# Performance work log

Measured on AMD Instinct MI355X. Metric: run time of the kernel, lower is better.

The kernel has to match this reference:

```python
import jax, jax.numpy as jnp
import numpy as np

B, T, C, H, TT = 8, 1024, 512, 8, 4  # batch, seq, n_embd, n_head, total_timestep
D = C // H


def setup_inputs() -> dict:
    key = jax.random.key(0)
    ks = jax.random.split(key, 4)
    s = 1.0 / np.sqrt(C)
    return {
        "x": jax.random.normal(ks[0], (B, T, C), jnp.float32),
        "padding_mask": jax.random.bernoulli(ks[1], 0.1, (TT, T)),  # bool
        "W_qkv": jax.random.normal(ks[2], (C, 3 * C), jnp.float32) * s,
        "b_qkv": jnp.zeros((3 * C,), jnp.float32),
        "W_proj": jax.random.normal(ks[3], (C, C), jnp.float32) * s,
        "b_proj": jnp.zeros((C,), jnp.float32),
    }


def reference(x, padding_mask, W_qkv, b_qkv, W_proj, b_proj):
    # fused QKV projection
    qkv = x @ W_qkv + b_qkv                       # [B,T,3C]
    q, k, v = jnp.split(qkv, 3, axis=-1)
    q = q.reshape(B, T, H, D)
    k = k.reshape(B, T, H, D)
    v = v.reshape(B, T, H, D)

    # mask: causal OR padding (True = attend), replicating torch semantics
    causal = jnp.tril(jnp.ones((T, T), bool))                 # [T,T]
    m = causal[None] | padding_mask[:, :, None]               # [TT,T,T]
    mask = jnp.broadcast_to(m[None], (B // TT, TT, T, T)).reshape(B, 1, T, T)

    scores = jnp.einsum("bqhd,bkhd->bhqk", q, k) * (1.0 / np.sqrt(D))
    scores = jnp.where(mask, scores, jnp.float32(-1e30))
    attn = jax.nn.softmax(scores, axis=-1)                    # [B,H,T,T]
    y = jnp.einsum("bhqk,bkhd->bqhd", attn, v).reshape(B, T, C)
    return y @ W_proj + b_proj
```

## Files before the change

### kernel.cpp

```cpp
#include <hip/hip_runtime.h>
#include <hip/hip_bf16.h>

#define BB 8
#define TT_ 4
#define TSEQ 1024
#define CEMB 512
#define NH 8
#define HD 64

typedef __attribute__((ext_vector_type(8))) short bf16x8;
typedef __attribute__((ext_vector_type(4))) float f32x4;
typedef __attribute__((ext_vector_type(16))) float f32x16;

#define AS1 __attribute__((address_space(1)))
#define AS3 __attribute__((address_space(3)))

__device__ __forceinline__ void gload_lds16(const void* g, void* l) {
  __builtin_amdgcn_global_load_lds((const AS1 unsigned int*)g, (AS3 unsigned int*)l, 16, 0, 0);
}

__device__ __forceinline__ short f2b(float f) {
  union { float f; unsigned u; } v; v.f = f;
  unsigned r = v.u + 0x7FFFu + ((v.u >> 16) & 1u);
  return (short)(r >> 16);
}

__device__ __forceinline__ unsigned pack2(float a, float b) {
  unsigned r;
  asm("v_cvt_pk_bf16_f32 %0, %1, %2" : "=v"(r) : "v"(a), "v"(b));
  return r;
}

__global__ __launch_bounds__(256) void k_prep(
    const float* __restrict__ x, short* __restrict__ xb,
    const float* __restrict__ w0, short* __restrict__ t0,
    const float* __restrict__ w1, short* __restrict__ t1)
{
  __shared__ float tsh[64][65];
  const int bid = blockIdx.x;

  if (bid < 2048) {
    const int i = bid * 256 + threadIdx.x;
    float4 v0 = ((const float4*)x)[i * 2];
    float4 v1 = ((const float4*)x)[i * 2 + 1];
    union { unsigned u[4]; bf16x8 v; } o;
    o.u[0] = pack2(v0.x, v0.y); o.u[1] = pack2(v0.z, v0.w);
    o.u[2] = pack2(v1.x, v1.y); o.u[3] = pack2(v1.z, v1.w);
    ((bf16x8*)xb)[i] = o.v;
    return;
  }

  const int z = (bid >= 2240);
  const int tile = z ? (bid - 2240) : (bid - 2048);
  const int ntx = z ? 8 : 24;
  const float* w = z ? w1 : w0;
  short* wt = z ? t1 : t0;
  const int N = z ? 512 : 1536, K = 512;
  const int tx = threadIdx.x & 15, ty = threadIdx.x >> 4;
  const int n0 = (tile % ntx) * 64, k0 = (tile / ntx) * 64;
#pragma unroll
  for (int i = 0; i < 4; ++i) {
    int kr = i * 16 + ty;
    float4 v = *(const float4*)&w[(size_t)(k0 + kr) * N + n0 + tx * 4];
    tsh[tx * 4 + 0][kr] = v.x; tsh[tx * 4 + 1][kr] = v.y;
    tsh[tx * 4 + 2][kr] = v.z; tsh[tx * 4 + 3][kr] = v.w;
  }
  __syncthreads();
#pragma unroll
  for (int i = 0; i < 4; ++i) {
    int nr = i * 16 + ty;
    short4 o;
    o.x = f2b(tsh[nr][tx * 4 + 0]); o.y = f2b(tsh[nr][tx * 4 + 1]);
    o.z = f2b(tsh[nr][tx * 4 + 2]); o.w = f2b(tsh[nr][tx * 4 + 3]);
    *(short4*)&wt[(size_t)(n0 + nr) * K + k0 + tx * 4] = o;
  }
}

__global__ __launch_bounds__(256) void k_gemm0(
    const short* __restrict__ A, const short* __restrict__ Bt,
    const float* __restrict__ bias,
    short* __restrict__ qb, short* __restrict__ kb, short* __restrict__ vtb,
    const void* __restrict__ pin, int* __restrict__ pme,
    int* __restrict__ perm, int* __restrict__ chunk_nkt)
{
  __shared__ short As[3][128 * 32];
  __shared__ short Bs[3][128 * 32];

  if (blockIdx.x == 768) {
    __shared__ int bad_f32, any_f32, bad_i32, any_i32, bad_u16, any_u16;
    if (threadIdx.x == 0) { bad_f32 = any_f32 = bad_i32 = any_i32 = bad_u16 = any_u16 = 0; }
    __syncthreads();
    const unsigned char* pb = (const unsigned char*)pin;
    const float* pf = (const float*)pin;
    const int* pi = (const int*)pin;
    const unsigned short* ph = (const unsigned short*)pin;
    for (int i = threadIdx.x; i < 1024; i += 256) {
      float fv = pf[i];
      if (fv != 0.0f && fv != 1.0f) bad_f32 = 1;
      if (fv == 1.0f) any_f32 = 1;
      int iv = pi[i];
      if (iv != 0 && iv != 1) bad_i32 = 1;
      if (iv == 1) any_i32 = 1;
    }
    for (int i = threadIdx.x; i < 2048; i += 256) {
      unsigned short hv = ph[i];
      if (hv != 0 && hv != 0x3F80u && hv != 0x3C00u) bad_u16 = 1;
      if (hv == 0x3F80u || hv == 0x3C00u) any_u16 = 1;
    }
    __syncthreads();
    int mode = 3;
    if (!bad_f32 && any_f32) mode = 0;
    else if (!bad_i32 && any_i32) mode = 1;
    else if (!bad_u16 && any_u16) mode = 2;
    for (int i = threadIdx.x; i < TT_ * TSEQ; i += 256) {
      int v;
      if (mode == 0)      v = (pf[i] != 0.0f);
      else if (mode == 1) v = (pi[i] != 0);
      else if (mode == 2) v = (ph[i] != 0);
      else                v = (pb[i] != 0);
      pme[i] = v;
    }
    __syncthreads();
    const int w = threadIdx.x >> 6, lane = threadIdx.x & 63;
    {
      const int* rowp = pme + w * 1024;
      unsigned long long bal[16];
      int npm = 0;
#pragma unroll
      for (int g = 0; g < 16; ++g) {
        bal[g] = __ballot(rowp[g * 64 + lane] != 0);
        npm += __popcll(bal[g]);
      }
      int off_non = 0, off_pm = 1024 - npm;
#pragma unroll
      for (int g = 0; g < 16; ++g) {
        unsigned long long m = bal[g];
        int below = __popcll(m & ((1ull << lane) - 1ull));
        int ispm = (int)((m >> lane) & 1ull);
        int pos = ispm ? (off_pm + below) : (off_non + lane - below);
        perm[w * 1024 + pos] = g * 64 + lane;
        int c = __popcll(m);
        off_pm += c; off_non += 64 - c;
      }
    }
    __syncthreads();
    {
      const int tt = w, c = (lane >> 3) & 7, seg = lane & 7;
      int mx = 0;
#pragma unroll
      for (int i = 0; i < 16; ++i) {
        int q = perm[tt * 1024 + c * 128 + seg * 16 + i];
        int need = pme[tt * 1024 + q] ? 16 : ((q >> 6) + 1);
        mx = mx > need ? mx : need;
      }
#pragma unroll
      for (int s = 1; s < 8; s <<= 1) {
        int o = __shfl_xor(mx, s, 64);
        mx = mx > o ? mx : o;
      }
      if (seg == 0) chunk_nkt[tt * 8 + c] = mx;
    }
    return;
  }

  const int tid = threadIdx.x, lane = tid & 63, w = tid >> 6;
  const int wm = w >> 1, wn = w & 1;
  const int idp = (blockIdx.x & 7) * 96 + (blockIdx.x >> 3);
  const int n0 = (idp % 12) * 128, m0 = (idp / 12) * 128;
  f32x4 acc[4][4] = {};
  const char* Abase = (const char*)A + (size_t)m0 * 1024;
  const char* Bbase = (const char*)Bt + (size_t)n0 * 1024;
  const int rowL = w * 16 + (lane >> 2);
  const int colB = (lane & 3) * 16;

  auto stage = [&](int buf, int k0) {
#pragma unroll
    for (int is = 0; is < 2; ++is) {
      int row = is * 64 + rowL;
      gload_lds16(Abase + (size_t)row * 1024 + (size_t)(k0 * 2 + colB),
                  (char*)As[buf] + is * 4096 + w * 1024);
      gload_lds16(Bbase + (size_t)row * 1024 + (size_t)(k0 * 2 + colB),
                  (char*)Bs[buf] + is * 4096 + w * 1024);
    }
  };

  stage(0, 0);
  stage(1, 32);
#pragma unroll
  for (int it = 0; it < 16; ++it) {
    if (it < 15) asm volatile("s_waitcnt vmcnt(4)\n\ts_barrier" ::: "memory");
    else         asm volatile("s_waitcnt vmcnt(0)\n\ts_barrier" ::: "memory");
    if (it + 2 < 16) stage((it + 2) % 3, (it + 2) * 32);
    const short* Ab = As[it % 3];
    const short* Bb = Bs[it % 3];
    bf16x8 a[4], bfr[4];
#pragma unroll
    for (int mf = 0; mf < 4; ++mf)
      a[mf] = *(const bf16x8*)&Ab[(wm * 64 + mf * 16 + (lane & 15)) * 32 + (lane >> 4) * 8];
#pragma unroll
    for (int nf = 0; nf < 4; ++nf)
      bfr[nf] = *(const bf16x8*)&Bb[(wn * 64 + nf * 16 + (lane & 15)) * 32 + (lane >> 4) * 8];
#pragma unroll
    for (int mf = 0; mf < 4; ++mf)
#pragma unroll
      for (int nf = 0; nf < 4; ++nf)
        acc[mf][nf] = __builtin_amdgcn_mfma_f32_16x16x32_bf16(a[mf], bfr[nf], acc[mf][nf], 0, 0, 0);
  }

#pragma unroll
  for (int nf = 0; nf < 4; ++nf) {
    const int n_g = n0 + wn * 64 + nf * 16 + (lane & 15);
    const float bv = bias[n_g];
    const int which = n_g >> 9;
    const int c = n_g & 511;
    const int h = c >> 6, d = c & 63;
    const float qsc = (which == 0) ? 0.18033688011112043f : 1.0f;
#pragma unroll
    for (int mf = 0; mf < 4; ++mf) {
      const int mb = m0 + wm * 64 + mf * 16 + ((lane >> 4) << 2);
      const int b = mb >> 10, t0 = mb & 1023;
      const int b8h = b * NH + h;
      if (which == 2) {
        short4 pk;
        pk.x = f2b(acc[mf][nf][0] + bv);
        pk.y = f2b(acc[mf][nf][1] + bv);
        pk.z = f2b(acc[mf][nf][2] + bv);
        pk.w = f2b(acc[mf][nf][3] + bv);
        *(short4*)&vtb[((size_t)b8h * HD + d) * TSEQ + t0] = pk;
      } else {
        short* dst = (which == 0) ? qb : kb;
        size_t base = ((size_t)b8h * TSEQ + t0) * HD + d;
#pragma unroll
        for (int r = 0; r < 4; ++r)
          dst[base + (size_t)r * HD] = f2b((acc[mf][nf][r] + bv) * qsc);
      }
    }
  }
}

__global__ __launch_bounds__(256) void k_gemm1(
    const short* __restrict__ A, const short* __restrict__ Bt,
    const float* __restrict__ bias, float* __restrict__ fout)
{
  __shared__ short As[3][64 * 32];
  __shared__ short Bs[3][128 * 32];
  const int tid = threadIdx.x, lane = tid & 63, w = tid >> 6;
  const int wm = w >> 1, wn = w & 1;
  const int idp = (blockIdx.x & 7) * 64 + (blockIdx.x >> 3);
  const int n0 = (idp & 3) * 128, m0 = (idp >> 2) * 64;
  f32x4 acc[2][4] = {};
  const char* Abase = (const char*)A + (size_t)m0 * 1024;
  const char* Bbase = (const char*)Bt + (size_t)n0 * 1024;
  const int rowL = tid >> 2;
  const int colB = (tid & 3) * 16;

  auto stage = [&](int buf, int k0) {
    gload_lds16(Abase + (size_t)rowL * 1024 + (size_t)(k0 * 2 + colB),
                (char*)As[buf] + w * 1024);
#pragma unroll
    for (int is = 0; is < 2; ++is) {
      int row = is * 64 + rowL;
      gload_lds16(Bbase + (size_t)row * 1024 + (size_t)(k0 * 2 + colB),
                  (char*)Bs[buf] + is * 4096 + w * 1024);
    }
  };

  stage(0, 0);
  stage(1, 32);
#pragma unroll
  for (int it = 0; it < 16; ++it) {
    if (it < 15) asm volatile("s_waitcnt vmcnt(3)\n\ts_barrier" ::: "memory");
    else         asm volatile("s_waitcnt vmcnt(0)\n\ts_barrier" ::: "memory");
    if (it + 2 < 16) stage((it + 2) % 3, (it + 2) * 32);
    const short* Ab = As[it % 3];
    const short* Bb = Bs[it % 3];
    bf16x8 a[2], bfr[4];
#pragma unroll
    for (int mf = 0; mf < 2; ++mf)
      a[mf] = *(const bf16x8*)&Ab[(wm * 32 + mf * 16 + (lane & 15)) * 32 + (lane >> 4) * 8];
#pragma unroll
    for (int nf = 0; nf < 4; ++nf)
      bfr[nf] = *(const bf16x8*)&Bb[(wn * 64 + nf * 16 + (lane & 15)) * 32 + (lane >> 4) * 8];
#pragma unroll
    for (int mf = 0; mf < 2; ++mf)
#pragma unroll
      for (int nf = 0; nf < 4; ++nf)
        acc[mf][nf] = __builtin_amdgcn_mfma_f32_16x16x32_bf16(a[mf], bfr[nf], acc[mf][nf], 0, 0, 0);
  }

#pragma unroll
  for (int nf = 0; nf < 4; ++nf) {
    const int n_g = n0 + wn * 64 + nf * 16 + (lane & 15);
    const float bv = bias[n_g];
#pragma unroll
    for (int mf = 0; mf < 2; ++mf) {
      const int mb = m0 + wm * 32 + mf * 16 + ((lane >> 4) << 2);
#pragma unroll
      for (int r = 0; r < 4; ++r)
        fout[(size_t)(mb + r) * 512 + n_g] = acc[mf][nf][r] + bv;
    }
  }
}

__device__ __forceinline__ void pv_step(
    f32x16 p, int sub, int hi, int lq, const char* Vsb, f32x16& o0, f32x16& o1)
{
  unsigned P2[8];
#pragma unroll
  for (int i = 0; i < 8; ++i) P2[i] = pack2(p[2 * i], p[2 * i + 1]);
  unsigned e0 = __shfl_xor(hi ? P2[0] : P2[2], 32, 64);
  unsigned e1 = __shfl_xor(hi ? P2[1] : P2[3], 32, 64);
  unsigned e2 = __shfl_xor(hi ? P2[4] : P2[6], 32, 64);
  unsigned e3 = __shfl_xor(hi ? P2[5] : P2[7], 32, 64);
  union { unsigned u[4]; bf16x8 v; } f0, f1;
  f0.u[0] = hi ? e0 : P2[0]; f0.u[1] = hi ? e1 : P2[1];
  f0.u[2] = hi ? P2[2] : e0; f0.u[3] = hi ? P2[3] : e1;
  f1.u[0] = hi ? e2 : P2[4]; f1.u[1] = hi ? e3 : P2[5];
  f1.u[2] = hi ? P2[6] : e2; f1.u[3] = hi ? P2[7] : e3;
  __builtin_amdgcn_s_setprio(1);
#pragma unroll
  for (int dt = 0; dt < 2; ++dt) {
    int row = dt * 32 + lq;
    bf16x8 v0 = *(const bf16x8*)(Vsb + row * 128 + ((4 * sub + hi) ^ (row & 7)) * 16);
    bf16x8 v1 = *(const bf16x8*)(Vsb + row * 128 + ((4 * sub + 2 + hi) ^ (row & 7)) * 16);
    f32x16& o = dt ? o1 : o0;
    o = __builtin_amdgcn_mfma_f32_32x32x16_bf16(v0, f0.v, o, 0, 0, 0);
    o = __builtin_amdgcn_mfma_f32_32x32x16_bf16(v1, f1.v, o, 0, 0, 0);
  }
  __builtin_amdgcn_s_setprio(0);
}

__global__ __launch_bounds__(512) void k_attn(
    const short* __restrict__ qg, const short* __restrict__ kg,
    const short* __restrict__ vtg, const int* __restrict__ pme,
    const int* __restrict__ perm, const int* __restrict__ chunk_nkt,
    short* __restrict__ yb)
{
  __shared__ char smem[65536];
  const int tid = threadIdx.x, lane = tid & 63, w = tid >> 6;
  const int g = w >> 2;
  const int hi = lane >> 5, lq = lane & 31;
  const int id = blockIdx.x;
  const int bh = id & 63, b = bh >> 3, h = bh & 7, tt = b & 3;
  const int p = id >> 6;
  const int chunk = (p < 4) ? (7 - p) : (p - 4);
  const char* Qb = (const char*)(qg + (size_t)bh * TSEQ * HD);
  const char* Kb = (const char*)(kg + (size_t)bh * TSEQ * HD);
  const char* Vb = (const char*)(vtg + (size_t)bh * HD * TSEQ);

  const int stg_row = ((w & 3) << 3) + (lane >> 3);
  const int stg_cl = (lane & 7) ^ ((lane >> 3) & 7);

  auto stage = [&](int buf, int kt) {
#pragma unroll
    for (int is = 0; is < 2; ++is) {
      int row = is * 32 + stg_row;
      gload_lds16(Kb + (size_t)(kt * 64 + row) * 128 + stg_cl * 16,
                  smem + buf * 8192 + is * 4096 + (w & 3) * 1024);
      gload_lds16(Vb + (size_t)row * 2048 + kt * 128 + stg_cl * 16,
                  smem + 32768 + buf * 8192 + is * 4096 + (w & 3) * 1024);
    }
  };

  const int nkt = chunk_nkt[tt * 8 + chunk];
  const int q_g = perm[tt * 1024 + chunk * 128 + (w & 3) * 32 + lq];
  const int pmrow = pme[tt * TSEQ + q_g];

  if (g < nkt) stage(g * 2, g);

  int wmq = q_g, wnq = q_g;
#pragma unroll
  for (int s = 1; s < 64; s <<= 1) {
    wmq = max(wmq, __shfl_xor(wmq, s, 64));
    wnq = min(wnq, __shfl_xor(wnq, s, 64));
  }
  const int whaspm = __any(pmrow != 0);

  bf16x8 qf[4];
#pragma unroll
  for (int dk = 0; dk < 4; ++dk)
    qf[dk] = *(const bf16x8*)(Qb + (size_t)q_g * 128 + dk * 32 + hi * 16);

  float mrun = -1e30f, lrun = 0.0f;
  f32x16 o0 = {}, o1 = {};

  const int niter = (nkt + 1) >> 1;
  for (int i = 0; i < niter; ++i) {
    asm volatile("s_waitcnt vmcnt(0)" ::: "memory");
    __builtin_amdgcn_s_barrier();
    const int kt = 2 * i + g;
    if (kt + 2 < nkt) stage(g * 2 + ((i + 1) & 1), kt + 2);

    const int kb_ = kt * 64;
    if (kt < nkt && (kb_ <= wmq || whaspm)) {
      const char* Ksb = smem + (g * 2 + (i & 1)) * 8192;
      const char* Vsb = smem + 32768 + (g * 2 + (i & 1)) * 8192;

      f32x16 s0 = {}, s1 = {};
      __builtin_amdgcn_s_setprio(1);
#pragma unroll
      for (int dk = 0; dk < 4; ++dk) {
        int row0 = lq, row1 = 32 + lq;
        bf16x8 kf0 = *(const bf16x8*)(Ksb + row0 * 128 + ((2 * dk + hi) ^ (row0 & 7)) * 16);
        bf16x8 kf1 = *(const bf16x8*)(Ksb + row1 * 128 + ((2 * dk + hi) ^ (row1 & 7)) * 16);
        s0 = __builtin_amdgcn_mfma_f32_32x32x16_bf16(kf0, qf[dk], s0, 0, 0, 0);
        s1 = __builtin_amdgcn_mfma_f32_32x32x16_bf16(kf1, qf[dk], s1, 0, 0, 0);
      }
      __builtin_amdgcn_s_setprio(0);

      if (kb_ + 63 <= wnq) {
      } else if (kb_ > wmq) {
#pragma unroll
        for (int r = 0; r < 16; ++r) {
          s0[r] = pmrow ? s0[r] : -1e30f;
          s1[r] = pmrow ? s1[r] : -1e30f;
        }
      } else {
#pragma unroll
        for (int r = 0; r < 16; ++r) {
          int crow = (r & 3) + 8 * (r >> 2) + 4 * hi;
          s0[r] = ((kb_ + crow <= q_g) || pmrow) ? s0[r] : -1e30f;
          s1[r] = ((kb_ + 32 + crow <= q_g) || pmrow) ? s1[r] : -1e30f;
        }
      }

      float tm[16];
#pragma unroll
      for (int r = 0; r < 16; ++r) tm[r] = fmaxf(s0[r], s1[r]);
#pragma unroll
      for (int st = 8; st >= 1; st >>= 1)
#pragma unroll
        for (int r = 0; r < 8; ++r)
          if (r < st) tm[r] = fmaxf(tm[r], tm[r + st]);
      float mx = fmaxf(tm[0], __shfl_xor(tm[0], 32, 64));
      if (!__all(mx <= mrun + 8.0f)) {
        float nm = fmaxf(mrun, mx);
        float sc = __builtin_amdgcn_exp2f(mrun - nm);
        lrun *= sc;
#pragma unroll
        for (int r = 0; r < 16; ++r) { o0[r] *= sc; o1[r] *= sc; }
        mrun = nm;
      }
#pragma unroll
      for (int r = 0; r < 16; ++r) s0[r] = __builtin_amdgcn_exp2f(s0[r] - mrun);
#pragma unroll
      for (int r = 0; r < 16; ++r) s1[r] = __builtin_amdgcn_exp2f(s1[r] - mrun);
      float ts[16];
#pragma unroll
      for (int r = 0; r < 16; ++r) ts[r] = s0[r] + s1[r];
#pragma unroll
      for (int st = 8; st >= 1; st >>= 1)
#pragma unroll
        for (int r = 0; r < 8; ++r)
          if (r < st) ts[r] = ts[r] + ts[r + st];
      lrun += ts[0] + __shfl_xor(ts[0], 32, 64);

      pv_step(s0, 0, hi, lq, Vsb, o0, o1);
      pv_step(s1, 1, hi, lq, Vsb, o0, o1);
    }
  }

  __syncthreads();
  float* mg = (float*)smem;
  const int idx = (w & 3) * 64 + lane;
  if (g == 1) {
    mg[idx * 34 + 0] = mrun;
    mg[idx * 34 + 1] = lrun;
#pragma unroll
    for (int j = 0; j < 16; ++j) mg[idx * 34 + 2 + j] = o0[j];
#pragma unroll
    for (int j = 0; j < 16; ++j) mg[idx * 34 + 18 + j] = o1[j];
  }
  __syncthreads();
  if (g == 0) {
    const float mB = mg[idx * 34 + 0], lB = mg[idx * 34 + 1];
    const float m = fmaxf(mrun, mB);
    const float wa = __builtin_amdgcn_exp2f(mrun - m);
    const float wb = __builtin_amdgcn_exp2f(mB - m);
    const float linv = 1.0f / (lrun * wa + lB * wb);
    const float fa = wa * linv, fb = wb * linv;
    short* yrow = yb + ((size_t)b * TSEQ + q_g) * CEMB + h * HD;
#pragma unroll
    for (int dt = 0; dt < 2; ++dt) {
      const f32x16& o = dt ? o1 : o0;
      const int ob = dt ? 18 : 2;
#pragma unroll
      for (int gg = 0; gg < 4; ++gg) {
        short4 pk;
        pk.x = f2b(o[4 * gg + 0] * fa + mg[idx * 34 + ob + 4 * gg + 0] * fb);
        pk.y = f2b(o[4 * gg + 1] * fa + mg[idx * 34 + ob + 4 * gg + 1] * fb);
        pk.z = f2b(o[4 * gg + 2] * fa + mg[idx * 34 + ob + 4 * gg + 2] * fb);
        pk.w = f2b(o[4 * gg + 3] * fa + mg[idx * 34 + ob + 4 * gg + 3] * fb);
        *(short4*)(yrow + dt * 32 + 8 * gg + 4 * hi) = pk;
      }
    }
  }
}

extern "C" void kernel_launch(void* const* d_in, const int* in_sizes, int n_in,
                              void* d_out, int out_size, void* d_ws, size_t ws_size,
                              hipStream_t stream) {
  const float* x     = (const float*)d_in[0];
  const void*  pmask = d_in[1];
  const float* Wqkv  = (const float*)d_in[2];
  const float* bqkv  = (const float*)d_in[3];
  const float* Wproj = (const float*)d_in[4];
  const float* bproj = (const float*)d_in[5];
  float* out = (float*)d_out;
  char* ws = (char*)d_ws;

  const size_t OFF_XB   = 0;
  const size_t OFF_WQT  = 8388608;
  const size_t OFF_WPT  = 9961472;
  const size_t OFF_Q    = 10485760;
  const size_t OFF_K    = 18874368;
  const size_t OFF_VT   = 27262976;
  const size_t OFF_Y    = 35651584;
  const size_t OFF_PM   = 44040192;
  const size_t OFF_PERM = 44056576;
  const size_t OFF_CNKT = 44072960;
  const size_t NEED     = 44073984;
  if (ws_size < NEED) return;

  short* xb  = (short*)(ws + OFF_XB);
  short* wqT = (short*)(ws + OFF_WQT);
  short* wpT = (short*)(ws + OFF_WPT);
  short* qb  = (short*)(ws + OFF_Q);
  short* kb  = (short*)(ws + OFF_K);
  short* vtb = (short*)(ws + OFF_VT);
  short* yb  = (short*)(ws + OFF_Y);
  int*   pme = (int*)(ws + OFF_PM);
  int*   prm = (int*)(ws + OFF_PERM);
  int*   cnk = (int*)(ws + OFF_CNKT);

  k_prep<<<dim3(2304), dim3(256), 0, stream>>>(x, xb, Wqkv, wqT, Wproj, wpT);
  k_gemm0<<<dim3(769), dim3(256), 0, stream>>>(xb, wqT, bqkv, qb, kb, vtb,
                                               pmask, pme, prm, cnk);
  k_attn<<<dim3(512), dim3(512), 0, stream>>>(qb, kb, vtb, pme, prm, cnk, yb);
  k_gemm1<<<dim3(512), dim3(256), 0, stream>>>(yb, wpT, bproj, out);
}
```

Measured before the change: 85.79 us.

## Move mask preprocessing to prep kernel, enlarge proj GEMM tile, stage attention output

Mask decoding, permutation and chunk-bound computation move from an extra block of the QKV GEMM into an extra block of the prep kernel, so the GEMM grid no longer carries a straggler block. The output projection GEMM switches from 64x128 to 128x128 tiles with half as many blocks, trading fewer blocks for more reuse per block. In attention, the chunk schedule becomes strictly descending, and outputs are staged in LDS then written as coalesced 16-byte rows using the permutation. The LDS staging adds a barrier, and the larger tiles leave fewer blocks to spread across CUs.

```diff
diff --git a/kernel.cpp b/kernel.cpp
--- a/kernel.cpp
+++ b/kernel.cpp
@@ -34,7 +34,9 @@
 __global__ __launch_bounds__(256) void k_prep(
     const float* __restrict__ x, short* __restrict__ xb,
     const float* __restrict__ w0, short* __restrict__ t0,
-    const float* __restrict__ w1, short* __restrict__ t1)
+    const float* __restrict__ w1, short* __restrict__ t1,
+    const void* __restrict__ pin, int* __restrict__ pme,
+    int* __restrict__ perm, int* __restrict__ chunk_nkt)
 {
   __shared__ float tsh[64][65];
   const int bid = blockIdx.x;
@@ -50,119 +52,117 @@
     return;
   }
 
-  const int z = (bid >= 2240);
-  const int tile = z ? (bid - 2240) : (bid - 2048);
-  const int ntx = z ? 8 : 24;
-  const float* w = z ? w1 : w0;
-  short* wt = z ? t1 : t0;
-  const int N = z ? 512 : 1536, K = 512;
-  const int tx = threadIdx.x & 15, ty = threadIdx.x >> 4;
-  const int n0 = (tile % ntx) * 64, k0 = (tile / ntx) * 64;
-#pragma unroll
-  for (int i = 0; i < 4; ++i) {
-    int kr = i * 16 + ty;
-    float4 v = *(const float4*)&w[(size_t)(k0 + kr) * N + n0 + tx * 4];
-    tsh[tx * 4 + 0][kr] = v.x; tsh[tx * 4 + 1][kr] = v.y;
-    tsh[tx * 4 + 2][kr] = v.z; tsh[tx * 4 + 3][kr] = v.w;
-  }
-  __syncthreads();
-#pragma unroll
-  for (int i = 0; i < 4; ++i) {
-    int nr = i * 16 + ty;
-    short4 o;
-    o.x = f2b(tsh[nr][tx * 4 + 0]); o.y = f2b(tsh[nr][tx * 4 + 1]);
-    o.z = f2b(tsh[nr][tx * 4 + 2]); o.w = f2b(tsh[nr][tx * 4 + 3]);
-    *(short4*)&wt[(size_t)(n0 + nr) * K + k0 + tx * 4] = o;
+  if (bid < 2304) {
+    const int z = (bid >= 2240);
+    const int tile = z ? (bid - 2240) : (bid - 2048);
+    const int ntx = z ? 8 : 24;
+    const float* w = z ? w1 : w0;
+    short* wt = z ? t1 : t0;
+    const int N = z ? 512 : 1536, K = 512;
+    const int tx = threadIdx.x & 15, ty = threadIdx.x >> 4;
+    const int n0 = (tile % ntx) * 64, k0 = (tile / ntx) * 64;
+#pragma unroll
+    for (int i = 0; i < 4; ++i) {
+      int kr = i * 16 + ty;
+      float4 v = *(const float4*)&w[(size_t)(k0 + kr) * N + n0 + tx * 4];
+      tsh[tx * 4 + 0][kr] = v.x; tsh[tx * 4 + 1][kr] = v.y;
+      tsh[tx * 4 + 2][kr] = v.z; tsh[tx * 4 + 3][kr] = v.w;
+    }
+    __syncthreads();
+#pragma unroll
+    for (int i = 0; i < 4; ++i) {
+      int nr = i * 16 + ty;
+      short4 o;
+      o.x = f2b(tsh[nr][tx * 4 + 0]); o.y = f2b(tsh[nr][tx * 4 + 1]);
+      o.z = f2b(tsh[nr][tx * 4 + 2]); o.w = f2b(tsh[nr][tx * 4 + 3]);
+      *(short4*)&wt[(size_t)(n0 + nr) * K + k0 + tx * 4] = o;
+    }
+    return;
+  }
+
+  __shared__ int bad_f32, any_f32, bad_i32, any_i32, bad_u16, any_u16;
+  if (threadIdx.x == 0) { bad_f32 = any_f32 = bad_i32 = any_i32 = bad_u16 = any_u16 = 0; }
+  __syncthreads();
+  const unsigned char* pb = (const unsigned char*)pin;
+  const float* pf = (const float*)pin;
+  const int* pi = (const int*)pin;
+  const unsigned short* ph = (const unsigned short*)pin;
+  for (int i = threadIdx.x; i < 1024; i += 256) {
+    float fv = pf[i];
+    if (fv != 0.0f && fv != 1.0f) bad_f32 = 1;
+    if (fv == 1.0f) any_f32 = 1;
+    int iv = pi[i];
+    if (iv != 0 && iv != 1) bad_i32 = 1;
+    if (iv == 1) any_i32 = 1;
+  }
+  for (int i = threadIdx.x; i < 2048; i += 256) {
+    unsigned short hv = ph[i];
+    if (hv != 0 && hv != 0x3F80u && hv != 0x3C00u) bad_u16 = 1;
+    if (hv == 0x3F80u || hv == 0x3C00u) any_u16 = 1;
+  }
+  __syncthreads();
+  int mode = 3;
+  if (!bad_f32 && any_f32) mode = 0;
+  else if (!bad_i32 && any_i32) mode = 1;
+  else if (!bad_u16 && any_u16) mode = 2;
+  for (int i = threadIdx.x; i < TT_ * TSEQ; i += 256) {
+    int v;
+    if (mode == 0)      v = (pf[i] != 0.0f);
+    else if (mode == 1) v = (pi[i] != 0);
+    else if (mode == 2) v = (ph[i] != 0);
+    else                v = (pb[i] != 0);
+    pme[i] = v;
+  }
+  __syncthreads();
+
+  const int w = threadIdx.x >> 6, lane = threadIdx.x & 63;
+  {
+    const int* rowp = pme + w * 1024;
+    unsigned long long bal[16];
+    int npm = 0;
+#pragma unroll
+    for (int g = 0; g < 16; ++g) {
+      bal[g] = __ballot(rowp[g * 64 + lane] != 0);
+      npm += __popcll(bal[g]);
+    }
+    int off_non = 0, off_pm = 1024 - npm;
+#pragma unroll
+    for (int g = 0; g < 16; ++g) {
+      unsigned long long m = bal[g];
+      int below = __popcll(m & ((1ull << lane) - 1ull));
+      int ispm = (int)((m >> lane) & 1ull);
+      int pos = ispm ? (off_pm + below) : (off_non + lane - below);
+      perm[w * 1024 + pos] = g * 64 + lane;
+      int c = __popcll(m);
+      off_pm += c; off_non += 64 - c;
+    }
+  }
+  __syncthreads();
+  {
+    const int tt = w, c = (lane >> 3) & 7, seg = lane & 7;
+    int mx = 0;
+#pragma unroll
+    for (int i = 0; i < 16; ++i) {
+      int q = perm[tt * 1024 + c * 128 + seg * 16 + i];
+      int need = pme[tt * 1024 + q] ? 16 : ((q >> 6) + 1);
+      mx = mx > need ? mx : need;
+    }
+#pragma unroll
+    for (int s = 1; s < 8; s <<= 1) {
+      int o = __shfl_xor(mx, s, 64);
+      mx = mx > o ? mx : o;
+    }
+    if (seg == 0) chunk_nkt[tt * 8 + c] = mx;
   }
 }
 
 __global__ __launch_bounds__(256) void k_gemm0(
     const short* __restrict__ A, const short* __restrict__ Bt,
     const float* __restrict__ bias,
-    short* __restrict__ qb, short* __restrict__ kb, short* __restrict__ vtb,
-    const void* __restrict__ pin, int* __restrict__ pme,
-    int* __restrict__ perm, int* __restrict__ chunk_nkt)
+    short* __restrict__ qb, short* __restrict__ kb, short* __restrict__ vtb)
 {
   __shared__ short As[3][128 * 32];
   __shared__ short Bs[3][128 * 32];
-
-  if (blockIdx.x == 768) {
-    __shared__ int bad_f32, any_f32, bad_i32, any_i32, bad_u16, any_u16;
-    if (threadIdx.x == 0) { bad_f32 = any_f32 = bad_i32 = any_i32 = bad_u16 = any_u16 = 0; }
-    __syncthreads();
-    const unsigned char* pb = (const unsigned char*)pin;
-    const float* pf = (const float*)pin;
-    const int* pi = (const int*)pin;
-    const unsigned short* ph = (const unsigned short*)pin;
-    for (int i = threadIdx.x; i < 1024; i += 256) {
-      float fv = pf[i];
-      if (fv != 0.0f && fv != 1.0f) bad_f32 = 1;
-      if (fv == 1.0f) any_f32 = 1;
-      int iv = pi[i];
-      if (iv != 0 && iv != 1) bad_i32 = 1;
-      if (iv == 1) any_i32 = 1;
-    }
-    for (int i = threadIdx.x; i < 2048; i += 256) {
-      unsigned short hv = ph[i];
-      if (hv != 0 && hv != 0x3F80u && hv != 0x3C00u) bad_u16 = 1;
-      if (hv == 0x3F80u || hv == 0x3C00u) any_u16 = 1;
-    }
-    __syncthreads();
-    int mode = 3;
-    if (!bad_f32 && any_f32) mode = 0;
-    else if (!bad_i32 && any_i32) mode = 1;
-    else if (!bad_u16 && any_u16) mode = 2;
-    for (int i = threadIdx.x; i < TT_ * TSEQ; i += 256) {
-      int v;
-      if (mode == 0)      v = (pf[i] != 0.0f);
-      else if (mode == 1) v = (pi[i] != 0);
-      else if (mode == 2) v = (ph[i] != 0);
-      else                v = (pb[i] != 0);
-      pme[i] = v;
-    }
-    __syncthreads();
-    const int w = threadIdx.x >> 6, lane = threadIdx.x & 63;
-    {
-      const int* rowp = pme + w * 1024;
-      unsigned long long bal[16];
-      int npm = 0;
-#pragma unroll
-      for (int g = 0; g < 16; ++g) {
-        bal[g] = __ballot(rowp[g * 64 + lane] != 0);
-        npm += __popcll(bal[g]);
-      }
-      int off_non = 0, off_pm = 1024 - npm;
-#pragma unroll
-      for (int g = 0; g < 16; ++g) {
-        unsigned long long m = bal[g];
-        int below = __popcll(m & ((1ull << lane) - 1ull));
-        int ispm = (int)((m >> lane) & 1ull);
-        int pos = ispm ? (off_pm + below) : (off_non + lane - below);
-        perm[w * 1024 + pos] = g * 64 + lane;
-        int c = __popcll(m);
-        off_pm += c; off_non += 64 - c;
-      }
-    }
-    __syncthreads();
-    {
-      const int tt = w, c = (lane >> 3) & 7, seg = lane & 7;
-      int mx = 0;
-#pragma unroll
-      for (int i = 0; i < 16; ++i) {
-        int q = perm[tt * 1024 + c * 128 + seg * 16 + i];
-        int need = pme[tt * 1024 + q] ? 16 : ((q >> 6) + 1);
-        mx = mx > need ? mx : need;
-      }
-#pragma unroll
-      for (int s = 1; s < 8; s <<= 1) {
-        int o = __shfl_xor(mx, s, 64);
-        mx = mx > o ? mx : o;
-      }
-      if (seg == 0) chunk_nkt[tt * 8 + c] = mx;
-    }
-    return;
-  }
-
   const int tid = threadIdx.x, lane = tid & 63, w = tid >> 6;
   const int wm = w >> 1, wn = w & 1;
   const int idp = (blockIdx.x & 7) * 96 + (blockIdx.x >> 3);
@@ -242,24 +242,24 @@
     const short* __restrict__ A, const short* __restrict__ Bt,
     const float* __restrict__ bias, float* __restrict__ fout)
 {
-  __shared__ short As[3][64 * 32];
+  __shared__ short As[3][128 * 32];
   __shared__ short Bs[3][128 * 32];
   const int tid = threadIdx.x, lane = tid & 63, w = tid >> 6;
   const int wm = w >> 1, wn = w & 1;
-  const int idp = (blockIdx.x & 7) * 64 + (blockIdx.x >> 3);
-  const int n0 = (idp & 3) * 128, m0 = (idp >> 2) * 64;
-  f32x4 acc[2][4] = {};
+  const int idp = (blockIdx.x & 7) * 32 + (blockIdx.x >> 3);
+  const int n0 = (idp % 4) * 128, m0 = (idp / 4) * 128;
+  f32x4 acc[4][4] = {};
   const char* Abase = (const char*)A + (size_t)m0 * 1024;
   const char* Bbase = (const char*)Bt + (size_t)n0 * 1024;
-  const int rowL = tid >> 2;
-  const int colB = (tid & 3) * 16;
+  const int rowL = w * 16 + (lane >> 2);
+  const int colB = (lane & 3) * 16;
 
   auto stage = [&](int buf, int k0) {
-    gload_lds16(Abase + (size_t)rowL * 1024 + (size_t)(k0 * 2 + colB),
-                (char*)As[buf] + w * 1024);
 #pragma unroll
     for (int is = 0; is < 2; ++is) {
       int row = is * 64 + rowL;
+      gload_lds16(Abase + (size_t)row * 1024 + (size_t)(k0 * 2 + colB),
+                  (char*)As[buf] + is * 4096 + w * 1024);
       gload_lds16(Bbase + (size_t)row * 1024 + (size_t)(k0 * 2 + colB),
                   (char*)Bs[buf] + is * 4096 + w * 1024);
     }
@@ -269,20 +269,20 @@
   stage(1, 32);
 #pragma unroll
   for (int it = 0; it < 16; ++it) {
-    if (it < 15) asm volatile("s_waitcnt vmcnt(3)\n\ts_barrier" ::: "memory");
+    if (it < 15) asm volatile("s_waitcnt vmcnt(4)\n\ts_barrier" ::: "memory");
     else         asm volatile("s_waitcnt vmcnt(0)\n\ts_barrier" ::: "memory");
     if (it + 2 < 16) stage((it + 2) % 3, (it + 2) * 32);
     const short* Ab = As[it % 3];
     const short* Bb = Bs[it % 3];
-    bf16x8 a[2], bfr[4];
-#pragma unroll
-    for (int mf = 0; mf < 2; ++mf)
-      a[mf] = *(const bf16x8*)&Ab[(wm * 32 + mf * 16 + (lane & 15)) * 32 + (lane >> 4) * 8];
+    bf16x8 a[4], bfr[4];
+#pragma unroll
+    for (int mf = 0; mf < 4; ++mf)
+      a[mf] = *(const bf16x8*)&Ab[(wm * 64 + mf * 16 + (lane & 15)) * 32 + (lane >> 4) * 8];
 #pragma unroll
     for (int nf = 0; nf < 4; ++nf)
       bfr[nf] = *(const bf16x8*)&Bb[(wn * 64 + nf * 16 + (lane & 15)) * 32 + (lane >> 4) * 8];
 #pragma unroll
-    for (int mf = 0; mf < 2; ++mf)
+    for (int mf = 0; mf < 4; ++mf)
 #pragma unroll
       for (int nf = 0; nf < 4; ++nf)
         acc[mf][nf] = __builtin_amdgcn_mfma_f32_16x16x32_bf16(a[mf], bfr[nf], acc[mf][nf], 0, 0, 0);
@@ -293,8 +293,8 @@
     const int n_g = n0 + wn * 64 + nf * 16 + (lane & 15);
     const float bv = bias[n_g];
 #pragma unroll
-    for (int mf = 0; mf < 2; ++mf) {
-      const int mb = m0 + wm * 32 + mf * 16 + ((lane >> 4) << 2);
+    for (int mf = 0; mf < 4; ++mf) {
+      const int mb = m0 + wm * 64 + mf * 16 + ((lane >> 4) << 2);
 #pragma unroll
       for (int r = 0; r < 4; ++r)
         fout[(size_t)(mb + r) * 512 + n_g] = acc[mf][nf][r] + bv;
@@ -342,8 +342,7 @@
   const int hi = lane >> 5, lq = lane & 31;
   const int id = blockIdx.x;
   const int bh = id & 63, b = bh >> 3, h = bh & 7, tt = b & 3;
-  const int p = id >> 6;
-  const int chunk = (p < 4) ? (7 - p) : (p - 4);
+  const int chunk = 7 - (id >> 6);
   const char* Qb = (const char*)(qg + (size_t)bh * TSEQ * HD);
   const char* Kb = (const char*)(kg + (size_t)bh * TSEQ * HD);
   const char* Vb = (const char*)(vtg + (size_t)bh * HD * TSEQ);
@@ -462,6 +461,7 @@
 
   __syncthreads();
   float* mg = (float*)smem;
+  short* ys = (short*)(smem + 36864);
   const int idx = (w & 3) * 64 + lane;
   if (g == 1) {
     mg[idx * 34 + 0] = mrun;
@@ -479,7 +479,7 @@
     const float wb = __builtin_amdgcn_exp2f(mB - m);
     const float linv = 1.0f / (lrun * wa + lB * wb);
     const float fa = wa * linv, fb = wb * linv;
-    short* yrow = yb + ((size_t)b * TSEQ + q_g) * CEMB + h * HD;
+    short* yl = ys + ((w & 3) * 32 + lq) * 72;
 #pragma unroll
     for (int dt = 0; dt < 2; ++dt) {
       const f32x16& o = dt ? o1 : o0;
@@ -491,9 +491,17 @@
         pk.y = f2b(o[4 * gg + 1] * fa + mg[idx * 34 + ob + 4 * gg + 1] * fb);
         pk.z = f2b(o[4 * gg + 2] * fa + mg[idx * 34 + ob + 4 * gg + 2] * fb);
         pk.w = f2b(o[4 * gg + 3] * fa + mg[idx * 34 + ob + 4 * gg + 3] * fb);
-        *(short4*)(yrow + dt * 32 + 8 * gg + 4 * hi) = pk;
+        *(short4*)(yl + dt * 32 + 8 * gg + 4 * hi) = pk;
       }
     }
+  }
+  __syncthreads();
+  {
+    const int row = tid >> 2, seg = tid & 3;
+    const int q_row = perm[tt * 1024 + chunk * 128 + row];
+    short* dst = yb + ((size_t)b * TSEQ + q_row) * CEMB + h * HD + seg * 16;
+    *(bf16x8*)dst = *(const bf16x8*)&ys[row * 72 + seg * 16];
+    *(bf16x8*)(dst + 8) = *(const bf16x8*)&ys[row * 72 + seg * 16 + 8];
   }
 }
 
@@ -533,9 +541,9 @@
   int*   prm = (int*)(ws + OFF_PERM);
   int*   cnk = (int*)(ws + OFF_CNKT);
 
-  k_prep<<<dim3(2304), dim3(256), 0, stream>>>(x, xb, Wqkv, wqT, Wproj, wpT);
-  k_gemm0<<<dim3(769), dim3(256), 0, stream>>>(xb, wqT, bqkv, qb, kb, vtb,
+  k_prep<<<dim3(2305), dim3(256), 0, stream>>>(x, xb, Wqkv, wqT, Wproj, wpT,
                                                pmask, pme, prm, cnk);
+  k_gemm0<<<dim3(768), dim3(256), 0, stream>>>(xb, wqT, bqkv, qb, kb, vtb);
   k_attn<<<dim3(512), dim3(512), 0, stream>>>(qb, kb, vtb, pme, prm, cnk, yb);
-  k_gemm1<<<dim3(512), dim3(256), 0, stream>>>(yb, wpT, bproj, out);
-}
+  k_gemm1<<<dim3(256), dim3(256), 0, stream>>>(yb, wpT, bproj, out);
+}
```

New measurement: 82.47 us. 3.9% less time.
